# Optimization experiments

Measured on AMD Instinct MI355X. Metric: run time of the kernel, lower is better.

The kernel has to match this reference:

```python
import jax, jax.numpy as jnp
import numpy as np

MODES, WIDTH, DEPTH, IN_F, OUT_F, HID = 8, 16, 3, 1, 1, 64


def setup_inputs() -> dict:
    key = jax.random.key(0)
    ks = jax.random.split(key, 12)
    B, H, W = 8, 512, 512
    scale = 1.0 / (WIDTH * WIDTH)
    inp = {
        'x': jax.random.normal(ks[0], (B, IN_F, H, W), dtype=jnp.float32),
        'fc0_w': jax.random.normal(ks[1], (IN_F, WIDTH), dtype=jnp.float32) * 0.5,
        'fc0_b': jax.random.normal(ks[2], (WIDTH,), dtype=jnp.float32) * 0.1,
        # complex spectral weights stored as real/imag parts, stacked over depth
        'spec_wr': jax.random.normal(ks[3], (DEPTH, WIDTH, WIDTH, MODES, MODES), dtype=jnp.float32) * scale,
        'spec_wi': jax.random.normal(ks[4], (DEPTH, WIDTH, WIDTH, MODES, MODES), dtype=jnp.float32) * scale,
        # 1x1 convs as [depth, out, in] matmuls + bias
        'conv_w': jax.random.normal(ks[5], (DEPTH, WIDTH, WIDTH), dtype=jnp.float32) * 0.25,
        'conv_b': jax.random.normal(ks[6], (DEPTH, WIDTH), dtype=jnp.float32) * 0.1,
        'fc1_w': jax.random.normal(ks[7], (WIDTH, HID), dtype=jnp.float32) * 0.25,
        'fc1_b': jax.random.normal(ks[8], (HID,), dtype=jnp.float32) * 0.1,
        'fc2_w': jax.random.normal(ks[9], (HID, OUT_F), dtype=jnp.float32) * 0.125,
        'fc2_b': jax.random.normal(ks[10], (OUT_F,), dtype=jnp.float32) * 0.1,
    }
    return inp


def _spectral_conv(x, w):
    # x: [B, Ci, H, W] real; w: [Ci, Co, m, m] complex
    B, C, H, W = x.shape
    m = w.shape[2]
    x_ft = jnp.fft.rfft2(x, norm='forward')  # [B, Ci, H, W//2+1]
    out_modes = jnp.einsum('bixy,ioxy->boxy', x_ft[:, :, :m, :m], w)
    out_ft = jnp.zeros((B, w.shape[1], H, W // 2 + 1), dtype=out_modes.dtype)
    out_ft = out_ft.at[:, :, :m, :m].set(out_modes)
    return jnp.fft.irfft2(out_ft, s=(H, W), norm='forward')


def reference(x, fc0_w, fc0_b, spec_wr, spec_wi, conv_w, conv_b, fc1_w, fc1_b, fc2_w, fc2_b):
    # lift: [B,C,H,W] -> channels-last linear -> [B,width,H,W]
    h = jnp.einsum('bchw,cd->bdhw', x, fc0_w) + fc0_b[None, :, None, None]
    for d in range(DEPTH):
        w_c = (spec_wr[d] + 1j * spec_wi[d]).astype(jnp.complex64)
        y = _spectral_conv(h, w_c)
        local = jnp.einsum('bchw,oc->bohw', h, conv_w[d]) + conv_b[d][None, :, None, None]
        h = y + local
    h = jnp.einsum('bchw,cd->bdhw', h, fc1_w) + fc1_b[None, :, None, None]
    h = jax.nn.relu(h)
    out = jnp.einsum('bchw,cd->bdhw', h, fc2_w) + fc2_b[None, :, None, None]
    return out
```

## Files before the change

kernel.cpp:

```cpp
#include <hip/hip_runtime.h>
#include <math.h>

#define NB 8
#define NH 512
#define NW 512
#define ANG512 0.01227184630308513f
#define SPEC_D 16384

__device__ __forceinline__ void treduce16(float* p, float* tb, float* dst, int tid) {
    #pragma unroll
    for (int j = 0; j < 16; ++j) p[j] += __shfl_xor(p[j], 1);
    if (!(tid & 1)) {
        const int s = tid >> 1;
        #pragma unroll
        for (int j = 0; j < 16; ++j) tb[s * 17 + j] = p[j];
    }
    __syncthreads();
    {
        const int q = tid >> 4, g = tid & 15;
        float v = 0.f;
        #pragma unroll
        for (int j = 0; j < 8; ++j) v += tb[(g + 16 * j) * 17 + q];
        #pragma unroll
        for (int m = 1; m < 16; m <<= 1) v += __shfl_xor(v, m, 16);
        if (g == 0) dst[q] = v;
    }
    __syncthreads();
}

__global__ __launch_bounds__(256) void k_rowdft(const float* __restrict__ x,
                                                float* __restrict__ R) {
    __shared__ float tb[128 * 17];
    __shared__ float red[16];
    const int tid = threadIdx.x;
    const int b = blockIdx.x >> 9;
    const int row = blockIdx.x & 511;
    const float* xr = x + ((size_t)(b * NH + row)) * NW;
    const float xa = xr[tid], xb = xr[tid + 256];
    const float a = xa + xb, d = xa - xb;

    float p[16];
    float c1, s1;
    __sincosf(ANG512 * (float)tid, &s1, &c1);
    p[0] = a;      p[8] = 0.f;
    p[1] = d * c1; p[9] = -d * s1;
    {
        const float c2k = 2.f * c1;
        float ckm = 1.f, skm = 0.f, ck = c1, sk = s1;
        #pragma unroll
        for (int k = 2; k < 8; ++k) {
            const float cn = fmaf(c2k, ck, -ckm);
            const float sn = fmaf(c2k, sk, -skm);
            ckm = ck; skm = sk; ck = cn; sk = sn;
            const float v = (k & 1) ? d : a;
            p[k] = v * ck;
            p[8 + k] = -v * sk;
        }
    }
    treduce16(p, tb, red, tid);
    if (tid < 16) R[((size_t)(b * NH + row)) * 16 + tid] = red[tid];
}

__global__ __launch_bounds__(256) void k_modes(
        const float* __restrict__ R,
        const float* __restrict__ spec_wr, const float* __restrict__ spec_wi,
        const float* __restrict__ conv_w, const float* __restrict__ conv_b,
        const float* __restrict__ fc0_w, const float* __restrict__ fc0_b,
        const float* __restrict__ fc1_w, const float* __restrict__ fc1_b,
        float* __restrict__ AH, float* __restrict__ gvec, float* __restrict__ Kvec) {
    __shared__ float Wr_s[3][16][16][8];
    __shared__ float Wi_s[3][16][16][8];
    __shared__ float tb[128 * 17];
    __shared__ float X2[16];
    __shared__ float Xr[16][8], Xi[16][8];
    __shared__ float Fr[16][8], Fi[16][8];
    __shared__ float Ar[16][8], Ai[16][8];
    __shared__ float Pm[2][256];
    __shared__ float fc1_s[1024];
    __shared__ float ps[64];

    const int tid = threadIdx.x;
    const int bb = blockIdx.x >> 3;
    const int kx = blockIdx.x & 7;

    {
        const int i = tid >> 4, o = tid & 15;
        #pragma unroll
        for (int d = 0; d < 3; ++d) {
            const size_t base = (size_t)d * SPEC_D + ((size_t)(i * 16 + o) * 64 + kx * 8);
            const float4* pr = (const float4*)(spec_wr + base);
            const float4* pi = (const float4*)(spec_wi + base);
            *(float4*)(&Wr_s[d][i][o][0]) = pr[0];
            *(float4*)(&Wr_s[d][i][o][4]) = pr[1];
            *(float4*)(&Wi_s[d][i][o][0]) = pi[0];
            *(float4*)(&Wi_s[d][i][o][4]) = pi[1];
        }
    }
    {
        const int o = tid >> 4, c = tid & 15;
        float s = 0.f;
        for (int k = 0; k < 16; ++k)
            s += conv_w[512 + o * 16 + k] * conv_w[256 + k * 16 + c];
        Pm[0][tid] = s;
    }
    Pm[1][tid] = conv_w[512 + tid];
    #pragma unroll
    for (int k = 0; k < 4; ++k) fc1_s[tid + k * 256] = fc1_w[tid + k * 256];

    float p[16];
    #pragma unroll
    for (int j = 0; j < 16; ++j) p[j] = 0.f;
    #pragma unroll
    for (int r2 = 0; r2 < 2; ++r2) {
        const int row = tid + r2 * 256;
        const float4* rp4 = (const float4*)(R + ((size_t)(bb * NH + row)) * 16);
        const float4 q0 = rp4[0], q1 = rp4[1], q2 = rp4[2], q3 = rp4[3];
        const float re[8] = {q0.x, q0.y, q0.z, q0.w, q1.x, q1.y, q1.z, q1.w};
        const float im[8] = {q2.x, q2.y, q2.z, q2.w, q3.x, q3.y, q3.z, q3.w};
        const int m = (kx * row) & 511;
        float cm, sm;
        __sincosf(ANG512 * (float)m, &sm, &cm);
        #pragma unroll
        for (int k = 0; k < 8; ++k) {
            p[k]     += re[k] * cm + im[k] * sm;
            p[8 + k] += im[k] * cm - re[k] * sm;
        }
    }
    treduce16(p, tb, X2, tid);

    const bool act = (tid < 128);
    const int o = tid >> 3, ky = tid & 7;
    if (act) {
        const float inv = 1.f / (512.f * 512.f);
        float xr0 = fc0_w[o] * X2[ky] * inv;
        float xi0 = fc0_w[o] * X2[8 + ky] * inv;
        if (kx == 0 && ky == 0) xr0 += fc0_b[o];
        Xr[o][ky] = xr0; Xi[o][ky] = xi0;
        Ar[o][ky] = 0.f; Ai[o][ky] = 0.f;
    }
    __syncthreads();

    for (int dd = 0; dd < 3; ++dd) {
        if (act) {
            float fr = 0.f, fi = 0.f;
            #pragma unroll
            for (int i = 0; i < 16; ++i) {
                const float wre = Wr_s[dd][i][o][ky];
                const float wim = Wi_s[dd][i][o][ky];
                const float xr0 = Xr[i][ky], xi0 = Xi[i][ky];
                fr += xr0 * wre - xi0 * wim;
                fi += xr0 * wim + xi0 * wre;
            }
            Fr[o][ky] = fr; Fi[o][ky] = fi;
        }
        __syncthreads();
        float xnr = 0.f, xni = 0.f;
        if (act) {
            float ar, ai;
            if (dd == 2) {
                ar = Fr[o][ky]; ai = Fi[o][ky];
            } else {
                ar = 0.f; ai = 0.f;
                #pragma unroll
                for (int c = 0; c < 16; ++c) {
                    const float pv = Pm[dd][o * 16 + c];
                    ar = fmaf(pv, Fr[c][ky], ar);
                    ai = fmaf(pv, Fi[c][ky], ai);
                }
            }
            Ar[o][ky] += ar; Ai[o][ky] += ai;
            if (dd < 2) {
                const float fr0 = Fr[o][ky], fi0 = Fi[o][ky];
                if (ky == 0) {
                    if (kx == 0) { xnr = fr0; xni = 0.f; }
                    else         { xnr = 0.5f * fr0; xni = 0.5f * fi0; }
                } else { xnr = fr0; xni = fi0; }
                #pragma unroll
                for (int c = 0; c < 16; ++c) {
                    const float cc = conv_w[dd * 256 + o * 16 + c];
                    xnr = fmaf(cc, Xr[c][ky], xnr);
                    xni = fmaf(cc, Xi[c][ky], xni);
                }
                if (kx == 0 && ky == 0) xnr += conv_b[dd * 16 + o];
            }
        }
        __syncthreads();
        if (act && dd < 2) { Xr[o][ky] = xnr; Xi[o][ky] = xni; }
        __syncthreads();
    }

    #pragma unroll
    for (int k2 = 0; k2 < 2; ++k2) {
        const int idx = tid + k2 * 256;
        const int hd = idx >> 3, ky2 = idx & 7;
        float ar = 0.f, ai = 0.f;
        #pragma unroll
        for (int c = 0; c < 16; ++c) {
            const float f = fc1_s[c * 64 + hd];
            ar = fmaf(f, Ar[c][ky2], ar);
            ai = fmaf(f, Ai[c][ky2], ai);
        }
        const float ck = (ky2 == 0) ? 1.f : 2.f;
        const size_t off = ((((size_t)(bb * 64 + hd)) * 8 + ky2) * 8 + kx) * 2;
        AH[off] = ck * ar;
        AH[off + 1] = ck * ai;
    }

    if (blockIdx.x == 0) {
        if (tid < 16) {
            float su = 0.f, sb = 0.f;
            for (int c = 0; c < 16; ++c) {
                su += conv_w[tid * 16 + c] * fc0_w[c];
                sb += conv_w[tid * 16 + c] * fc0_b[c];
            }
            ps[tid] = su; ps[16 + tid] = sb;
        }
        __syncthreads();
        if (tid < 16) {
            float dv = 0.f, ev = conv_b[32 + tid];
            for (int k = 0; k < 16; ++k) {
                dv += Pm[0][tid * 16 + k] * ps[k];
                ev += Pm[0][tid * 16 + k] * (ps[16 + k] + conv_b[k]);
                ev += conv_w[512 + tid * 16 + k] * conv_b[16 + k];
            }
            ps[32 + tid] = dv; ps[48 + tid] = ev;
        }
        __syncthreads();
        if (tid < 64) {
            float g = 0.f, K = fc1_b[tid];
            for (int c = 0; c < 16; ++c) {
                g = fmaf(fc1_w[c * 64 + tid], ps[32 + c], g);
                K = fmaf(fc1_w[c * 64 + tid], ps[48 + c], K);
            }
            gvec[tid] = g; Kvec[tid] = K;
        }
    }
}

__global__ __launch_bounds__(256, 4) void k_head(
        const float* __restrict__ x, const float* __restrict__ AH,
        const float* __restrict__ gvec, const float* __restrict__ Kvec,
        const float* __restrict__ fc2_w, const float* __restrict__ fc2_b,
        float* __restrict__ out) {
    __shared__ float WHr[4][512];
    __shared__ float WHi[4][512];

    const int tid = threadIdx.x;
    const int b = blockIdx.x >> 7;
    const int rp = blockIdx.x & 127;
    const int rl = tid >> 6;
    const int row = rp * 4 + rl;
    const int w0 = tid & 63;

    const float* xp = x + ((size_t)(b * NH + row)) * NW + w0;
    float xv[8];
    #pragma unroll
    for (int j = 0; j < 8; ++j) xv[j] = xp[j * 64];

    {
        float c1, s1;
        __sincosf(ANG512 * (float)row, &s1, &c1);
        float ctr[8], str[8];
        ctr[0] = 1.f; str[0] = 0.f; ctr[1] = c1; str[1] = s1;
        const float c2k = 2.f * c1;
        #pragma unroll
        for (int k = 2; k < 8; ++k) {
            ctr[k] = fmaf(c2k, ctr[k - 1], -ctr[k - 2]);
            str[k] = fmaf(c2k, str[k - 1], -str[k - 2]);
        }
        #pragma unroll
        for (int j = 0; j < 8; ++j) {
            const int idx = w0 + j * 64;
            const int hd = idx >> 3, ky = idx & 7;
            const float4* ap = (const float4*)(AH + ((size_t)(b * 64 + hd) * 8 + ky) * 16);
            const float4 a0 = ap[0], a1 = ap[1], a2 = ap[2], a3 = ap[3];
            float wr = a0.x, wi = a0.y;
            wr = fmaf(a0.z, ctr[1], wr); wr = fmaf(-a0.w, str[1], wr);
            wi = fmaf(a0.z, str[1], wi); wi = fmaf(a0.w, ctr[1], wi);
            wr = fmaf(a1.x, ctr[2], wr); wr = fmaf(-a1.y, str[2], wr);
            wi = fmaf(a1.x, str[2], wi); wi = fmaf(a1.y, ctr[2], wi);
            wr = fmaf(a1.z, ctr[3], wr); wr = fmaf(-a1.w, str[3], wr);
            wi = fmaf(a1.z, str[3], wi); wi = fmaf(a1.w, ctr[3], wi);
            wr = fmaf(a2.x, ctr[4], wr); wr = fmaf(-a2.y, str[4], wr);
            wi = fmaf(a2.x, str[4], wi); wi = fmaf(a2.y, ctr[4], wi);
            wr = fmaf(a2.z, ctr[5], wr); wr = fmaf(-a2.w, str[5], wr);
            wi = fmaf(a2.z, str[5], wi); wi = fmaf(a2.w, ctr[5], wi);
            wr = fmaf(a3.x, ctr[6], wr); wr = fmaf(-a3.y, str[6], wr);
            wi = fmaf(a3.x, str[6], wi); wi = fmaf(a3.y, ctr[6], wi);
            wr = fmaf(a3.z, ctr[7], wr); wr = fmaf(-a3.w, str[7], wr);
            wi = fmaf(a3.z, str[7], wi); wi = fmaf(a3.w, ctr[7], wi);
            if (ky == 0) wr += Kvec[hd];
            WHr[rl][idx] = wr;
            WHi[rl][idx] = wi;
        }
    }
    __syncthreads();

    {
        float c1, s1;
        __sincosf(ANG512 * (float)w0, &s1, &c1);
        float ct[8], st[8];
        ct[0] = 1.f; st[0] = 0.f; ct[1] = c1; st[1] = s1;
        const float c2k = 2.f * c1;
        #pragma unroll
        for (int k = 2; k < 8; ++k) {
            ct[k] = fmaf(c2k, ct[k - 1], -ct[k - 2]);
            st[k] = fmaf(c2k, st[k - 1], -st[k - 2]);
        }
        const float r2c = 0.70710678118654752f;
        const float* WR = &WHr[rl][0];
        const float* WI = &WHi[rl][0];
        const float fc2b = fc2_b[0];
        float acc[8];
        #pragma unroll
        for (int j = 0; j < 8; ++j) acc[j] = fc2b;

        #pragma unroll 4
        for (int hd = 0; hd < 64; ++hd) {
            const float4* r4 = (const float4*)(WR + hd * 8);
            const float4 wa = r4[0], wb = r4[1];
            const float4* i4 = (const float4*)(WI + hd * 8);
            const float4 va = i4[0], vb = i4[1];
            const float tr0 = wa.x;
            const float tr1 = wa.y * ct[1] - va.y * st[1];
            const float ti1 = wa.y * st[1] + va.y * ct[1];
            const float tr2 = wa.z * ct[2] - va.z * st[2];
            const float ti2 = wa.z * st[2] + va.z * ct[2];
            const float tr3 = wa.w * ct[3] - va.w * st[3];
            const float ti3 = wa.w * st[3] + va.w * ct[3];
            const float tr4 = wb.x * ct[4] - vb.x * st[4];
            const float tr5 = wb.y * ct[5] - vb.y * st[5];
            const float ti5 = wb.y * st[5] + vb.y * ct[5];
            const float tr6 = wb.z * ct[6] - vb.z * st[6];
            const float ti6 = wb.z * st[6] + vb.z * ct[6];
            const float tr7 = wb.w * ct[7] - vb.w * st[7];
            const float ti7 = wb.w * st[7] + vb.w * ct[7];

            const float gh = gvec[hd];
            const float w2 = fc2_w[hd];

            const float A0 = tr0 + tr4, A2 = tr2 + tr6;
            const float E = A0 + A2, D = A0 - A2;
            const float B13 = (tr1 + tr5) + (tr3 + tr7);
            const float U = (ti1 + ti5) - (ti3 + ti7);
            const float s0 = fmaf(gh, xv[0], E + B13);
            const float s2 = fmaf(gh, xv[2], D - U);
            const float s4 = fmaf(gh, xv[4], E - B13);
            const float s6 = fmaf(gh, xv[6], D + U);
            acc[0] = fmaf(fmaxf(s0, 0.f), w2, acc[0]);
            acc[2] = fmaf(fmaxf(s2, 0.f), w2, acc[2]);
            acc[4] = fmaf(fmaxf(s4, 0.f), w2, acc[4]);
            acc[6] = fmaf(fmaxf(s6, 0.f), w2, acc[6]);

            const float P = tr0 - tr4, Q = ti6 - ti2;
            const float E2 = P + Q, D2 = P - Q;
            const float B2 = r2c * (((tr1 - ti1) - (tr5 - ti5)) + ((tr7 + ti7) - (tr3 + ti3)));
            const float U2 = r2c * (((tr1 + ti1) - (tr5 + ti5)) - ((tr3 - ti3) + (ti7 - tr7)));
            const float s1p = fmaf(gh, xv[1], E2 + B2);
            const float s3p = fmaf(gh, xv[3], D2 - U2);
            const float s5p = fmaf(gh, xv[5], E2 - B2);
            const float s7p = fmaf(gh, xv[7], D2 + U2);
            acc[1] = fmaf(fmaxf(s1p, 0.f), w2, acc[1]);
            acc[3] = fmaf(fmaxf(s3p, 0.f), w2, acc[3]);
            acc[5] = fmaf(fmaxf(s5p, 0.f), w2, acc[5]);
            acc[7] = fmaf(fmaxf(s7p, 0.f), w2, acc[7]);
        }
        float* op = out + ((size_t)(b * NH + row)) * NW + w0;
        #pragma unroll
        for (int j = 0; j < 8; ++j) op[j * 64] = acc[j];
    }
}

extern "C" void kernel_launch(void* const* d_in, const int* in_sizes, int n_in,
                              void* d_out, int out_size, void* d_ws, size_t ws_size,
                              hipStream_t stream) {
    const float* x       = (const float*)d_in[0];
    const float* fc0_w   = (const float*)d_in[1];
    const float* fc0_b   = (const float*)d_in[2];
    const float* spec_wr = (const float*)d_in[3];
    const float* spec_wi = (const float*)d_in[4];
    const float* conv_w  = (const float*)d_in[5];
    const float* conv_b  = (const float*)d_in[6];
    const float* fc1_w   = (const float*)d_in[7];
    const float* fc1_b   = (const float*)d_in[8];
    const float* fc2_w   = (const float*)d_in[9];
    const float* fc2_b   = (const float*)d_in[10];
    float* outp = (float*)d_out;

    char* ws = (char*)d_ws;
    float* R  = (float*)ws;
    float* AH = (float*)(ws + 262144);
    float* gv = (float*)(ws + 524288);
    float* Kv = (float*)(ws + 524288 + 256);

    k_rowdft<<<NB * NH, 256, 0, stream>>>(x, R);
    k_modes<<<NB * 8, 256, 0, stream>>>(R, spec_wr, spec_wi, conv_w, conv_b,
                                        fc0_w, fc0_b, fc1_w, fc1_b, AH, gv, Kv);
    k_head<<<NB * 128, 256, 0, stream>>>(x, AH, gv, Kv, fc2_w, fc2_b, outp);
}
```

Baseline: 143.7 us.

## Fuse column DFT into row-DFT kernel via atomic accumulation of modes

Each row-DFT block now applies the column twiddles for all 8 kx modes itself and atomically accumulates its contribution into a small global mode buffer, which a new zero kernel clears first. k_modes just reads the 16 values it needs, dropping its 512-row reduction and the intermediate R buffer. This takes the serial column reduction off the 64-block k_modes kernel, at the cost of heavy atomic contention (512 rows adding to each address) and one extra launch.

Result: slower. 160.9 us (+12.0%).

```diff
diff --git a/kernel.cpp b/kernel.cpp
--- a/kernel.cpp
+++ b/kernel.cpp
@@ -28,8 +28,12 @@
     __syncthreads();
 }
 
+__global__ void k_zero(float* __restrict__ X2g) {
+    X2g[(blockIdx.x << 8) + threadIdx.x] = 0.f;
+}
+
 __global__ __launch_bounds__(256) void k_rowdft(const float* __restrict__ x,
-                                                float* __restrict__ R) {
+                                                float* __restrict__ X2g) {
     __shared__ float tb[128 * 17];
     __shared__ float red[16];
     const int tid = threadIdx.x;
@@ -58,11 +62,20 @@
         }
     }
     treduce16(p, tb, red, tid);
-    if (tid < 16) R[((size_t)(b * NH + row)) * 16 + tid] = red[tid];
+
+    if (tid < 128) {
+        const int kx = tid >> 4, q = tid & 15;
+        const int m = (kx * row) & 511;
+        float cm, sm;
+        __sincosf(ANG512 * (float)m, &sm, &cm);
+        const float v = (q < 8) ? (red[q] * cm + red[q + 8] * sm)
+                                : (red[q] * cm - red[q - 8] * sm);
+        atomicAdd(X2g + ((size_t)((b << 3) + kx) * 16 + q), v);
+    }
 }
 
 __global__ __launch_bounds__(256) void k_modes(
-        const float* __restrict__ R,
+        const float* __restrict__ X2g,
         const float* __restrict__ spec_wr, const float* __restrict__ spec_wi,
         const float* __restrict__ conv_w, const float* __restrict__ conv_b,
         const float* __restrict__ fc0_w, const float* __restrict__ fc0_b,
@@ -70,7 +83,6 @@
         float* __restrict__ AH, float* __restrict__ gvec, float* __restrict__ Kvec) {
     __shared__ float Wr_s[3][16][16][8];
     __shared__ float Wi_s[3][16][16][8];
-    __shared__ float tb[128 * 17];
     __shared__ float X2[16];
     __shared__ float Xr[16][8], Xi[16][8];
     __shared__ float Fr[16][8], Fi[16][8];
@@ -106,27 +118,8 @@
     Pm[1][tid] = conv_w[512 + tid];
     #pragma unroll
     for (int k = 0; k < 4; ++k) fc1_s[tid + k * 256] = fc1_w[tid + k * 256];
-
-    float p[16];
-    #pragma unroll
-    for (int j = 0; j < 16; ++j) p[j] = 0.f;
-    #pragma unroll
-    for (int r2 = 0; r2 < 2; ++r2) {
-        const int row = tid + r2 * 256;
-        const float4* rp4 = (const float4*)(R + ((size_t)(bb * NH + row)) * 16);
-        const float4 q0 = rp4[0], q1 = rp4[1], q2 = rp4[2], q3 = rp4[3];
-        const float re[8] = {q0.x, q0.y, q0.z, q0.w, q1.x, q1.y, q1.z, q1.w};
-        const float im[8] = {q2.x, q2.y, q2.z, q2.w, q3.x, q3.y, q3.z, q3.w};
-        const int m = (kx * row) & 511;
-        float cm, sm;
-        __sincosf(ANG512 * (float)m, &sm, &cm);
-        #pragma unroll
-        for (int k = 0; k < 8; ++k) {
-            p[k]     += re[k] * cm + im[k] * sm;
-            p[8 + k] += im[k] * cm - re[k] * sm;
-        }
-    }
-    treduce16(p, tb, X2, tid);
+    if (tid < 16) X2[tid] = X2g[((size_t)((bb << 3) + kx)) * 16 + tid];
+    __syncthreads();
 
     const bool act = (tid < 128);
     const int o = tid >> 3, ky = tid & 7;
@@ -388,13 +381,14 @@
     float* outp = (float*)d_out;
 
     char* ws = (char*)d_ws;
-    float* R  = (float*)ws;
-    float* AH = (float*)(ws + 262144);
-    float* gv = (float*)(ws + 524288);
-    float* Kv = (float*)(ws + 524288 + 256);
-
-    k_rowdft<<<NB * NH, 256, 0, stream>>>(x, R);
-    k_modes<<<NB * 8, 256, 0, stream>>>(R, spec_wr, spec_wi, conv_w, conv_b,
+    float* X2g = (float*)ws;
+    float* AH  = (float*)(ws + 4096);
+    float* gv  = (float*)(ws + 4096 + 262144);
+    float* Kv  = (float*)(ws + 4096 + 262144 + 256);
+
+    k_zero<<<4, 256, 0, stream>>>(X2g);
+    k_rowdft<<<NB * NH, 256, 0, stream>>>(x, X2g);
+    k_modes<<<NB * 8, 256, 0, stream>>>(X2g, spec_wr, spec_wi, conv_w, conv_b,
                                         fc0_w, fc0_b, fc1_w, fc1_b, AH, gv, Kv);
     k_head<<<NB * 128, 256, 0, stream>>>(x, AH, gv, Kv, fc2_w, fc2_b, outp);
 }
```

## Fuse three stages into one cooperative kernel with grid syncs

Applied to the files above, without the earlier changes.

Merges the row-DFT, mode-mixing and head kernels into a single cooperative launch of 1024 blocks separated by grid-wide syncs, with a three-launch fallback if the cooperative launch fails. The row DFT now uses one wavefront per row with shuffle-only reductions instead of a 256-thread block with a shared-memory transpose. The mode stage reads spectral weights straight from global memory instead of staging them in LDS. The aim is to cut launch gaps and LDS and barrier overhead. In exchange it takes on grid-sync cost, idles most blocks during the 64-block middle phase, and needs all 1024 blocks to be co-resident.

After: 301.3 us. 2.1x slower.

```diff
diff --git a/kernel.cpp b/kernel.cpp
--- a/kernel.cpp
+++ b/kernel.cpp
@@ -1,5 +1,8 @@
 #include <hip/hip_runtime.h>
+#include <hip/hip_cooperative_groups.h>
 #include <math.h>
+
+namespace cg = cooperative_groups;
 
 #define NB 8
 #define NH 512
@@ -7,44 +10,27 @@
 #define ANG512 0.01227184630308513f
 #define SPEC_D 16384
 
-__device__ __forceinline__ void treduce16(float* p, float* tb, float* dst, int tid) {
-    #pragma unroll
-    for (int j = 0; j < 16; ++j) p[j] += __shfl_xor(p[j], 1);
-    if (!(tid & 1)) {
-        const int s = tid >> 1;
-        #pragma unroll
-        for (int j = 0; j < 16; ++j) tb[s * 17 + j] = p[j];
-    }
-    __syncthreads();
-    {
-        const int q = tid >> 4, g = tid & 15;
-        float v = 0.f;
-        #pragma unroll
-        for (int j = 0; j < 8; ++j) v += tb[(g + 16 * j) * 17 + q];
-        #pragma unroll
-        for (int m = 1; m < 16; m <<= 1) v += __shfl_xor(v, m, 16);
-        if (g == 0) dst[q] = v;
-    }
-    __syncthreads();
-}
-
-__global__ __launch_bounds__(256) void k_rowdft(const float* __restrict__ x,
-                                                float* __restrict__ R) {
-    __shared__ float tb[128 * 17];
-    __shared__ float red[16];
-    const int tid = threadIdx.x;
-    const int b = blockIdx.x >> 9;
-    const int row = blockIdx.x & 511;
+__device__ __forceinline__ void phaseA(const float* __restrict__ x,
+                                       float* __restrict__ R) {
+    const int wid = (blockIdx.x << 2) + (threadIdx.x >> 6);
+    const int lane = threadIdx.x & 63;
+    const int b = wid >> 9, row = wid & 511;
     const float* xr = x + ((size_t)(b * NH + row)) * NW;
-    const float xa = xr[tid], xb = xr[tid + 256];
-    const float a = xa + xb, d = xa - xb;
 
     float p[16];
-    float c1, s1;
-    __sincosf(ANG512 * (float)tid, &s1, &c1);
-    p[0] = a;      p[8] = 0.f;
-    p[1] = d * c1; p[9] = -d * s1;
-    {
+    #pragma unroll
+    for (int j = 0; j < 16; ++j) p[j] = 0.f;
+
+    #pragma unroll
+    for (int j = 0; j < 4; ++j) {
+        const int w = lane + (j << 6);
+        const float xa = xr[w], xb = xr[w + 256];
+        const float a = xa + xb, d = xa - xb;
+        float c1, s1;
+        __sincosf(ANG512 * (float)w, &s1, &c1);
+        p[0] += a;
+        p[1] = fmaf(d, c1, p[1]);
+        p[9] = fmaf(-d, s1, p[9]);
         const float c2k = 2.f * c1;
         float ckm = 1.f, skm = 0.f, ck = c1, sk = s1;
         #pragma unroll
@@ -53,57 +39,50 @@
             const float sn = fmaf(c2k, sk, -skm);
             ckm = ck; skm = sk; ck = cn; sk = sn;
             const float v = (k & 1) ? d : a;
-            p[k] = v * ck;
-            p[8 + k] = -v * sk;
-        }
-    }
-    treduce16(p, tb, red, tid);
-    if (tid < 16) R[((size_t)(b * NH + row)) * 16 + tid] = red[tid];
-}
-
-__global__ __launch_bounds__(256) void k_modes(
+            p[k]     = fmaf(v, ck, p[k]);
+            p[8 + k] = fmaf(-v, sk, p[8 + k]);
+        }
+    }
+    #pragma unroll
+    for (int m = 1; m < 64; m <<= 1) {
+        #pragma unroll
+        for (int j = 0; j < 16; ++j) p[j] += __shfl_xor(p[j], m);
+    }
+    if (lane < 16) R[((size_t)wid) * 16 + lane] = p[lane];
+}
+
+__device__ __forceinline__ void phaseB(
         const float* __restrict__ R,
         const float* __restrict__ spec_wr, const float* __restrict__ spec_wi,
         const float* __restrict__ conv_w, const float* __restrict__ conv_b,
         const float* __restrict__ fc0_w, const float* __restrict__ fc0_b,
         const float* __restrict__ fc1_w, const float* __restrict__ fc1_b,
-        float* __restrict__ AH, float* __restrict__ gvec, float* __restrict__ Kvec) {
-    __shared__ float Wr_s[3][16][16][8];
-    __shared__ float Wi_s[3][16][16][8];
-    __shared__ float tb[128 * 17];
-    __shared__ float X2[16];
-    __shared__ float Xr[16][8], Xi[16][8];
-    __shared__ float Fr[16][8], Fi[16][8];
-    __shared__ float Ar[16][8], Ai[16][8];
-    __shared__ float Pm[2][256];
-    __shared__ float fc1_s[1024];
-    __shared__ float ps[64];
+        float* __restrict__ AH, float* __restrict__ gvec, float* __restrict__ Kvec,
+        float* sm, int bid) {
+    float* partial = sm;
+    float* X2      = sm + 64;
+    float* Xr      = sm + 80;
+    float* Xi      = sm + 208;
+    float* Fr      = sm + 336;
+    float* Fi      = sm + 464;
+    float* Ar      = sm + 592;
+    float* Ai      = sm + 720;
+    float* Pm      = sm + 848;
+    float* fc1_s   = sm + 1360;
+    float* ps      = sm + 2384;
 
     const int tid = threadIdx.x;
-    const int bb = blockIdx.x >> 3;
-    const int kx = blockIdx.x & 7;
-
-    {
-        const int i = tid >> 4, o = tid & 15;
-        #pragma unroll
-        for (int d = 0; d < 3; ++d) {
-            const size_t base = (size_t)d * SPEC_D + ((size_t)(i * 16 + o) * 64 + kx * 8);
-            const float4* pr = (const float4*)(spec_wr + base);
-            const float4* pi = (const float4*)(spec_wi + base);
-            *(float4*)(&Wr_s[d][i][o][0]) = pr[0];
-            *(float4*)(&Wr_s[d][i][o][4]) = pr[1];
-            *(float4*)(&Wi_s[d][i][o][0]) = pi[0];
-            *(float4*)(&Wi_s[d][i][o][4]) = pi[1];
-        }
-    }
+    const int bb = bid >> 3;
+    const int kx = bid & 7;
+
     {
         const int o = tid >> 4, c = tid & 15;
         float s = 0.f;
         for (int k = 0; k < 16; ++k)
             s += conv_w[512 + o * 16 + k] * conv_w[256 + k * 16 + c];
-        Pm[0][tid] = s;
-    }
-    Pm[1][tid] = conv_w[512 + tid];
+        Pm[tid] = s;
+    }
+    Pm[256 + tid] = conv_w[512 + tid];
     #pragma unroll
     for (int k = 0; k < 4; ++k) fc1_s[tid + k * 256] = fc1_w[tid + k * 256];
 
@@ -118,15 +97,24 @@
         const float re[8] = {q0.x, q0.y, q0.z, q0.w, q1.x, q1.y, q1.z, q1.w};
         const float im[8] = {q2.x, q2.y, q2.z, q2.w, q3.x, q3.y, q3.z, q3.w};
         const int m = (kx * row) & 511;
-        float cm, sm;
-        __sincosf(ANG512 * (float)m, &sm, &cm);
+        float cm, sm2;
+        __sincosf(ANG512 * (float)m, &sm2, &cm);
         #pragma unroll
         for (int k = 0; k < 8; ++k) {
-            p[k]     += re[k] * cm + im[k] * sm;
-            p[8 + k] += im[k] * cm - re[k] * sm;
-        }
-    }
-    treduce16(p, tb, X2, tid);
+            p[k]     += re[k] * cm + im[k] * sm2;
+            p[8 + k] += im[k] * cm - re[k] * sm2;
+        }
+    }
+    #pragma unroll
+    for (int m = 1; m < 64; m <<= 1) {
+        #pragma unroll
+        for (int j = 0; j < 16; ++j) p[j] += __shfl_xor(p[j], m);
+    }
+    if ((tid & 63) < 16) partial[(tid >> 6) * 16 + (tid & 63)] = p[tid & 63];
+    __syncthreads();
+    if (tid < 16)
+        X2[tid] = partial[tid] + partial[16 + tid] + partial[32 + tid] + partial[48 + tid];
+    __syncthreads();
 
     const bool act = (tid < 128);
     const int o = tid >> 3, ky = tid & 7;
@@ -135,42 +123,44 @@
         float xr0 = fc0_w[o] * X2[ky] * inv;
         float xi0 = fc0_w[o] * X2[8 + ky] * inv;
         if (kx == 0 && ky == 0) xr0 += fc0_b[o];
-        Xr[o][ky] = xr0; Xi[o][ky] = xi0;
-        Ar[o][ky] = 0.f; Ai[o][ky] = 0.f;
+        Xr[o * 8 + ky] = xr0; Xi[o * 8 + ky] = xi0;
+        Ar[o * 8 + ky] = 0.f; Ai[o * 8 + ky] = 0.f;
     }
     __syncthreads();
 
     for (int dd = 0; dd < 3; ++dd) {
         if (act) {
             float fr = 0.f, fi = 0.f;
+            const float* wrp = spec_wr + (size_t)dd * SPEC_D + o * 64 + kx * 8 + ky;
+            const float* wip = spec_wi + (size_t)dd * SPEC_D + o * 64 + kx * 8 + ky;
             #pragma unroll
             for (int i = 0; i < 16; ++i) {
-                const float wre = Wr_s[dd][i][o][ky];
-                const float wim = Wi_s[dd][i][o][ky];
-                const float xr0 = Xr[i][ky], xi0 = Xi[i][ky];
+                const float wre = wrp[i * 1024];
+                const float wim = wip[i * 1024];
+                const float xr0 = Xr[i * 8 + ky], xi0 = Xi[i * 8 + ky];
                 fr += xr0 * wre - xi0 * wim;
                 fi += xr0 * wim + xi0 * wre;
             }
-            Fr[o][ky] = fr; Fi[o][ky] = fi;
+            Fr[o * 8 + ky] = fr; Fi[o * 8 + ky] = fi;
         }
         __syncthreads();
         float xnr = 0.f, xni = 0.f;
         if (act) {
             float ar, ai;
             if (dd == 2) {
-                ar = Fr[o][ky]; ai = Fi[o][ky];
+                ar = Fr[o * 8 + ky]; ai = Fi[o * 8 + ky];
             } else {
                 ar = 0.f; ai = 0.f;
                 #pragma unroll
                 for (int c = 0; c < 16; ++c) {
-                    const float pv = Pm[dd][o * 16 + c];
-                    ar = fmaf(pv, Fr[c][ky], ar);
-                    ai = fmaf(pv, Fi[c][ky], ai);
+                    const float pv = Pm[dd * 256 + o * 16 + c];
+                    ar = fmaf(pv, Fr[c * 8 + ky], ar);
+                    ai = fmaf(pv, Fi[c * 8 + ky], ai);
                 }
             }
-            Ar[o][ky] += ar; Ai[o][ky] += ai;
+            Ar[o * 8 + ky] += ar; Ai[o * 8 + ky] += ai;
             if (dd < 2) {
-                const float fr0 = Fr[o][ky], fi0 = Fi[o][ky];
+                const float fr0 = Fr[o * 8 + ky], fi0 = Fi[o * 8 + ky];
                 if (ky == 0) {
                     if (kx == 0) { xnr = fr0; xni = 0.f; }
                     else         { xnr = 0.5f * fr0; xni = 0.5f * fi0; }
@@ -178,14 +168,14 @@
                 #pragma unroll
                 for (int c = 0; c < 16; ++c) {
                     const float cc = conv_w[dd * 256 + o * 16 + c];
-                    xnr = fmaf(cc, Xr[c][ky], xnr);
-                    xni = fmaf(cc, Xi[c][ky], xni);
+                    xnr = fmaf(cc, Xr[c * 8 + ky], xnr);
+                    xni = fmaf(cc, Xi[c * 8 + ky], xni);
                 }
                 if (kx == 0 && ky == 0) xnr += conv_b[dd * 16 + o];
             }
         }
         __syncthreads();
-        if (act && dd < 2) { Xr[o][ky] = xnr; Xi[o][ky] = xni; }
+        if (act && dd < 2) { Xr[o * 8 + ky] = xnr; Xi[o * 8 + ky] = xni; }
         __syncthreads();
     }
 
@@ -197,8 +187,8 @@
         #pragma unroll
         for (int c = 0; c < 16; ++c) {
             const float f = fc1_s[c * 64 + hd];
-            ar = fmaf(f, Ar[c][ky2], ar);
-            ai = fmaf(f, Ai[c][ky2], ai);
+            ar = fmaf(f, Ar[c * 8 + ky2], ar);
+            ai = fmaf(f, Ai[c * 8 + ky2], ai);
         }
         const float ck = (ky2 == 0) ? 1.f : 2.f;
         const size_t off = ((((size_t)(bb * 64 + hd)) * 8 + ky2) * 8 + kx) * 2;
@@ -206,7 +196,7 @@
         AH[off + 1] = ck * ai;
     }
 
-    if (blockIdx.x == 0) {
+    if (bid == 0) {
         if (tid < 16) {
             float su = 0.f, sb = 0.f;
             for (int c = 0; c < 16; ++c) {
@@ -219,8 +209,8 @@
         if (tid < 16) {
             float dv = 0.f, ev = conv_b[32 + tid];
             for (int k = 0; k < 16; ++k) {
-                dv += Pm[0][tid * 16 + k] * ps[k];
-                ev += Pm[0][tid * 16 + k] * (ps[16 + k] + conv_b[k]);
+                dv += Pm[tid * 16 + k] * ps[k];
+                ev += Pm[tid * 16 + k] * (ps[16 + k] + conv_b[k]);
                 ev += conv_w[512 + tid * 16 + k] * conv_b[16 + k];
             }
             ps[32 + tid] = dv; ps[48 + tid] = ev;
@@ -237,13 +227,13 @@
     }
 }
 
-__global__ __launch_bounds__(256, 4) void k_head(
+__device__ __forceinline__ void phaseC(
         const float* __restrict__ x, const float* __restrict__ AH,
         const float* __restrict__ gvec, const float* __restrict__ Kvec,
         const float* __restrict__ fc2_w, const float* __restrict__ fc2_b,
-        float* __restrict__ out) {
-    __shared__ float WHr[4][512];
-    __shared__ float WHi[4][512];
+        float* __restrict__ out, float* sm) {
+    float* WHr = sm;
+    float* WHi = sm + 2048;
 
     const int tid = threadIdx.x;
     const int b = blockIdx.x >> 7;
@@ -290,8 +280,8 @@
             wr = fmaf(a3.z, ctr[7], wr); wr = fmaf(-a3.w, str[7], wr);
             wi = fmaf(a3.z, str[7], wi); wi = fmaf(a3.w, ctr[7], wi);
             if (ky == 0) wr += Kvec[hd];
-            WHr[rl][idx] = wr;
-            WHi[rl][idx] = wi;
+            WHr[rl * 512 + idx] = wr;
+            WHi[rl * 512 + idx] = wi;
         }
     }
     __syncthreads();
@@ -308,8 +298,8 @@
             st[k] = fmaf(c2k, st[k - 1], -st[k - 2]);
         }
         const float r2c = 0.70710678118654752f;
-        const float* WR = &WHr[rl][0];
-        const float* WI = &WHi[rl][0];
+        const float* WR = WHr + rl * 512;
+        const float* WI = WHi + rl * 512;
         const float fc2b = fc2_b[0];
         float acc[8];
         #pragma unroll
@@ -371,6 +361,53 @@
     }
 }
 
+__global__ __launch_bounds__(256, 4) void k_fused(
+        const float* __restrict__ x,
+        const float* __restrict__ spec_wr, const float* __restrict__ spec_wi,
+        const float* __restrict__ conv_w, const float* __restrict__ conv_b,
+        const float* __restrict__ fc0_w, const float* __restrict__ fc0_b,
+        const float* __restrict__ fc1_w, const float* __restrict__ fc1_b,
+        const float* __restrict__ fc2_w, const float* __restrict__ fc2_b,
+        float* __restrict__ R, float* __restrict__ AH,
+        float* __restrict__ gvec, float* __restrict__ Kvec,
+        float* __restrict__ out) {
+    __shared__ __align__(16) float sm[4096];
+
+    phaseA(x, R);
+    cg::this_grid().sync();
+    if (blockIdx.x < 64)
+        phaseB(R, spec_wr, spec_wi, conv_w, conv_b, fc0_w, fc0_b,
+               fc1_w, fc1_b, AH, gvec, Kvec, sm, blockIdx.x);
+    cg::this_grid().sync();
+    phaseC(x, AH, gvec, Kvec, fc2_w, fc2_b, out, sm);
+}
+
+__global__ __launch_bounds__(256, 4) void k_pA(const float* __restrict__ x,
+                                               float* __restrict__ R) {
+    phaseA(x, R);
+}
+
+__global__ __launch_bounds__(256) void k_pB(
+        const float* __restrict__ R,
+        const float* __restrict__ spec_wr, const float* __restrict__ spec_wi,
+        const float* __restrict__ conv_w, const float* __restrict__ conv_b,
+        const float* __restrict__ fc0_w, const float* __restrict__ fc0_b,
+        const float* __restrict__ fc1_w, const float* __restrict__ fc1_b,
+        float* __restrict__ AH, float* __restrict__ gvec, float* __restrict__ Kvec) {
+    __shared__ __align__(16) float sm[2448];
+    phaseB(R, spec_wr, spec_wi, conv_w, conv_b, fc0_w, fc0_b,
+           fc1_w, fc1_b, AH, gvec, Kvec, sm, blockIdx.x);
+}
+
+__global__ __launch_bounds__(256, 4) void k_pC(
+        const float* __restrict__ x, const float* __restrict__ AH,
+        const float* __restrict__ gvec, const float* __restrict__ Kvec,
+        const float* __restrict__ fc2_w, const float* __restrict__ fc2_b,
+        float* __restrict__ out) {
+    __shared__ __align__(16) float sm[4096];
+    phaseC(x, AH, gvec, Kvec, fc2_w, fc2_b, out, sm);
+}
+
 extern "C" void kernel_launch(void* const* d_in, const int* in_sizes, int n_in,
                               void* d_out, int out_size, void* d_ws, size_t ws_size,
                               hipStream_t stream) {
@@ -393,8 +430,18 @@
     float* gv = (float*)(ws + 524288);
     float* Kv = (float*)(ws + 524288 + 256);
 
-    k_rowdft<<<NB * NH, 256, 0, stream>>>(x, R);
-    k_modes<<<NB * 8, 256, 0, stream>>>(R, spec_wr, spec_wi, conv_w, conv_b,
-                                        fc0_w, fc0_b, fc1_w, fc1_b, AH, gv, Kv);
-    k_head<<<NB * 128, 256, 0, stream>>>(x, AH, gv, Kv, fc2_w, fc2_b, outp);
-}
+    void* args[] = {(void*)&x, (void*)&spec_wr, (void*)&spec_wi,
+                    (void*)&conv_w, (void*)&conv_b, (void*)&fc0_w, (void*)&fc0_b,
+                    (void*)&fc1_w, (void*)&fc1_b, (void*)&fc2_w, (void*)&fc2_b,
+                    (void*)&R, (void*)&AH, (void*)&gv, (void*)&Kv, (void*)&outp};
+    hipError_t err = hipLaunchCooperativeKernel((const void*)k_fused,
+                                                dim3(1024), dim3(256),
+                                                args, 0, stream);
+    if (err != hipSuccess) {
+        (void)hipGetLastError();
+        k_pA<<<1024, 256, 0, stream>>>(x, R);
+        k_pB<<<64, 256, 0, stream>>>(R, spec_wr, spec_wi, conv_w, conv_b,
+                                     fc0_w, fc0_b, fc1_w, fc1_b, AH, gv, Kv);
+        k_pC<<<1024, 256, 0, stream>>>(x, AH, gv, Kv, fc2_w, fc2_b, outp);
+    }
+}
```
